# Kernel tuning notes

Hardware: AMD Instinct MI355X
Metric: run time of the kernel (lower is better)

## Reference

```python
import jax, jax.numpy as jnp
import numpy as np

B, S, DIN = 2, 2048, 1024
H = 16
DK = 1024   # dim_key_query_all
DV = 1024   # dim_value_all
DOUT = 1024
HEAD_SIZE = DK / H  # attention_head_size (float division in source)
LN_EPS = 1e-5


def setup_inputs() -> dict:
    key = jax.random.key(0)
    ks = jax.random.split(key, 12)
    s_in = 1.0 / np.sqrt(DIN)
    s_dv = 1.0 / np.sqrt(DV)
    return {
        "hidden_states": jax.random.normal(ks[0], (B, S, DIN), jnp.float32),
        "Wq": jax.random.uniform(ks[1], (DK, DIN), jnp.float32, -s_in, s_in),
        "Wk": jax.random.uniform(ks[2], (DK, DIN), jnp.float32, -s_in, s_in),
        "Wcb": jax.random.uniform(ks[3], (H, DIN), jnp.float32, -s_in, s_in),
        "Wv": jax.random.uniform(ks[4], (DV, DIN), jnp.float32, -s_in, s_in),
        "bv": jax.random.uniform(ks[5], (DV,), jnp.float32, -s_in, s_in),
        "mixing": 0.2 * jax.random.normal(ks[6], (H, DK), jnp.float32),
        "Wd": jax.random.uniform(ks[7], (DOUT, DV), jnp.float32, -s_dv, s_dv),
        "bd": jax.random.uniform(ks[8], (DOUT,), jnp.float32, -s_dv, s_dv),
        "gamma": jnp.ones((DV,), jnp.float32),
        "beta": jnp.zeros((DV,), jnp.float32),
    }


def reference(hidden_states, Wq, Wk, Wcb, Wv, bv, mixing, Wd, bd, gamma, beta):
    x = hidden_states  # [B, S, DIN]; self-attention: from == to
    q = jnp.einsum('bsd,kd->bsk', x, Wq)  # [B,S,DK]
    k = jnp.einsum('bsd,kd->bsk', x, Wk)  # [B,S,DK]
    # scores[b,h,i,j] = sum_c q[b,i,c]*mixing[h,c]*k[b,j,c]
    scores = jnp.einsum('bic,hc,bjc->bhij', q, mixing, k)
    cb = jnp.einsum('bjd,hd->bhj', x, Wcb)  # content bias [B,H,S]
    scores = scores + cb[:, :, None, :]
    scores = scores / jnp.sqrt(jnp.asarray(HEAD_SIZE, scores.dtype))
    probs = jax.nn.softmax(scores, axis=-1)  # dropout p=0.0 -> identity
    v = jnp.einsum('bsd,vd->bsv', x, Wv) + bv  # [B,S,DV]
    v = v.reshape(B, S, H, DV // H)
    ctx = jnp.einsum('bhij,bjhv->bihv', probs, v).reshape(B, S, DV)
    out = jnp.einsum('bsv,ov->bso', ctx, Wd) + bd
    res = x + out
    mu = jnp.mean(res, axis=-1, keepdims=True)
    var = jnp.var(res, axis=-1, keepdims=True)
    out = (res - mu) * jax.lax.rsqrt(var + LN_EPS) * gamma + beta
    return (out,)
```

## Files before the change

### kernel.cpp

```cpp
#include <hip/hip_runtime.h>
#include <cstddef>
#include <cstdint>

#define B_    2
#define S_    2048
#define DIN_  1024
#define H_    16
#define DK_   1024
#define DV_   1024
#define DH_   64
#define DOUT_ 1024
#define M_    (B_ * S_)

typedef __attribute__((ext_vector_type(8)))  short short8;
typedef __attribute__((ext_vector_type(4)))  float float4v;
typedef __attribute__((ext_vector_type(16))) float float16v;
typedef _Float16 half8v __attribute__((ext_vector_type(8)));

__device__ __forceinline__ float bf16s_to_f(short s) {
  union { unsigned int u; float f; } cv;
  cv.u = ((unsigned int)(unsigned short)s) << 16;
  return cv.f;
}
__device__ __forceinline__ short f_to_bf16s(float f) {
  union { float f; unsigned int u; } cv;
  cv.f = f;
  unsigned int u = cv.u + 0x7FFFu + ((cv.u >> 16) & 1u);
  return (short)(u >> 16);
}
__device__ __forceinline__ short f_to_f16s(float f) {
  union { _Float16 h; short s; } cv;
  cv.h = (_Float16)f;
  return cv.s;
}
__device__ __forceinline__ unsigned pkrtz_u32(float a, float b) {
  union { __fp16 __attribute__((ext_vector_type(2))) h2; unsigned u; } cv;
  cv.h2 = __builtin_amdgcn_cvt_pkrtz(a, b);
  return cv.u;
}
__device__ __forceinline__ void gll16(const void* g, void* l) {
  __builtin_amdgcn_global_load_lds(
      (const __attribute__((address_space(1))) unsigned int*)g,
      (__attribute__((address_space(3))) unsigned int*)l, 16, 0, 0);
}

__global__ __launch_bounds__(256) void cast_kernel(const float* __restrict__ in,
                                                   short* __restrict__ out, int n4) {
  int i = blockIdx.x * 256 + threadIdx.x;
  if (i >= n4) return;
  float4 v = ((const float4*)in)[i];
  union { ushort4 u; short s[4]; } o;
  o.s[0] = f_to_bf16s(v.x); o.s[1] = f_to_bf16s(v.y);
  o.s[2] = f_to_bf16s(v.z); o.s[3] = f_to_bf16s(v.w);
  ((ushort4*)out)[i] = o.u;
}

__global__ __launch_bounds__(256) void cb_kernel(const float* __restrict__ x,
                                                 const float* __restrict__ Wcb,
                                                 float* __restrict__ CBs) {
  __shared__ float xs[DIN_];
  const int row = blockIdx.x;
  const int tid = threadIdx.x;
  #pragma unroll
  for (int it = 0; it < 4; ++it)
    xs[tid + it * 256] = x[(size_t)row * DIN_ + tid + it * 256];
  __syncthreads();
  const int lane = tid & 63, w = tid >> 6;
  const float SC = 0.125f * 1.44269504088896f;
  #pragma unroll
  for (int hh = 0; hh < 4; ++hh) {
    const int hidx = w * 4 + hh;
    float p = 0.f;
    for (int c = lane; c < DIN_; c += 64)
      p += xs[c] * Wcb[(size_t)hidx * DIN_ + c];
    #pragma unroll
    for (int mk = 1; mk < 64; mk <<= 1) p += __shfl_xor(p, mk);
    if (lane == 0) {
      const int bb = row / S_, ss = row % S_;
      CBs[((size_t)bb * H_ + hidx) * S_ + ss] = p * SC;
    }
  }
}

__global__ __launch_bounds__(256, 2) void gemm_nt(
    const short* __restrict__ A, const short* __restrict__ Bw,
    const float* __restrict__ bias, const float* __restrict__ resid,
    short* __restrict__ outb, float* __restrict__ outf, int mode) {
  const int KD = 1024, ND = 1024;
  __shared__ short As[64][136];
  __shared__ short Bs[64][136];
  const int tid  = threadIdx.x;
  const int lane = tid & 63;
  const int w    = tid >> 6;
  const int quad = lane >> 4;
  const int l16  = lane & 15;
  const int m0   = blockIdx.y * 64;
  const int n0   = blockIdx.x * 64;
  const int wm   = (w >> 1) * 32;
  const int wn   = (w & 1) * 32;
  const int srow = tid >> 2;
  const int sseg = (tid & 3) * 32;

  const float4v zero = {0.f, 0.f, 0.f, 0.f};
  float4v acc[2][2];
  acc[0][0] = zero; acc[0][1] = zero; acc[1][0] = zero; acc[1][1] = zero;

  for (int k0 = 0; k0 < KD; k0 += 128) {
    short8 ar[4], br[4];
    #pragma unroll
    for (int c = 0; c < 4; ++c) {
      ar[c] = *(const short8*)(A  + (size_t)(m0 + srow) * KD + k0 + sseg + c * 8);
      br[c] = *(const short8*)(Bw + (size_t)(n0 + srow) * KD + k0 + sseg + c * 8);
    }
    __syncthreads();
    #pragma unroll
    for (int c = 0; c < 4; ++c) {
      *(short8*)&As[srow][sseg + c * 8] = ar[c];
      *(short8*)&Bs[srow][sseg + c * 8] = br[c];
    }
    __syncthreads();
    #pragma unroll
    for (int ks = 0; ks < 4; ++ks) {
      short8 af0 = *(short8*)&As[wm + l16][ks * 32 + quad * 8];
      short8 af1 = *(short8*)&As[wm + 16 + l16][ks * 32 + quad * 8];
      short8 bg0 = *(short8*)&Bs[wn + l16][ks * 32 + quad * 8];
      short8 bg1 = *(short8*)&Bs[wn + 16 + l16][ks * 32 + quad * 8];
      acc[0][0] = __builtin_amdgcn_mfma_f32_16x16x32_bf16(af0, bg0, acc[0][0], 0, 0, 0);
      acc[0][1] = __builtin_amdgcn_mfma_f32_16x16x32_bf16(af0, bg1, acc[0][1], 0, 0, 0);
      acc[1][0] = __builtin_amdgcn_mfma_f32_16x16x32_bf16(af1, bg0, acc[1][0], 0, 0, 0);
      acc[1][1] = __builtin_amdgcn_mfma_f32_16x16x32_bf16(af1, bg1, acc[1][1], 0, 0, 0);
    }
  }

  #pragma unroll
  for (int mt = 0; mt < 2; ++mt)
    #pragma unroll
    for (int nt = 0; nt < 2; ++nt)
      #pragma unroll
      for (int r = 0; r < 4; ++r) {
        int row = m0 + wm + mt * 16 + quad * 4 + r;
        int col = n0 + wn + nt * 16 + l16;
        float v = acc[mt][nt][r];
        if (mode == 1 || mode == 5) v += bias[col];
        if (mode == 2)
          outf[(size_t)row * ND + col] = v + bias[col] + resid[(size_t)row * ND + col];
        else if (mode == 5) {
          int bb = row >> 11, ss = row & 2047;
          outb[((size_t)bb * DV_ + col) * S_ + ss] = f_to_f16s(v);
        } else if (mode == 4)
          outb[(size_t)row * ND + col] = f_to_f16s(v);
        else
          outb[(size_t)row * ND + col] = f_to_bf16s(v);
      }
}

__global__ __launch_bounds__(256, 2) void attn_kernel(
    const short* __restrict__ Qf, const short* __restrict__ Kf,
    const short* __restrict__ Vtf, const float* __restrict__ mixing,
    const float* __restrict__ CBs, short* __restrict__ ctxb) {
  __shared__ __align__(16) short KsF[2 * 128 * 64];
  __shared__ __align__(16) short Vt[64][136];
  __shared__ __align__(16) short mix_s[DK_];
  __shared__ float cb_s[128];

  const int tid  = threadIdx.x;
  const int lane = tid & 63;
  const int l32  = lane & 31;
  const int l1   = lane >> 5;
  const int w    = tid >> 6;

  const int F    = blockIdx.x;
  const int xcd  = F & 7, rest = F >> 3;
  const int b    = xcd >> 2;
  const int h    = (xcd & 3) * 4 + (rest & 3);
  const int i0   = (rest >> 2) * 128;

  const float SC = 0.125f * 1.44269504088896f;
  for (int c = tid; c < DK_; c += 256) {
    union { _Float16 h; short s; } cv;
    cv.h = (_Float16)(mixing[(size_t)h * DK_ + c] * SC);
    mix_s[c] = cv.s;
  }

  const int iq = i0 + w * 32 + l32;
  const short* qptr  = Qf + ((size_t)b * S_ + iq) * DK_;
  const short* kbase = Kf + (size_t)b * S_ * DK_;
  const short* vtb   = Vtf + ((size_t)b * DV_ + h * DH_) * S_;
  const float* cbp   = CBs + ((size_t)b * H_ + h) * S_;

  float16v accS[4], accO[2];
  #pragma unroll
  for (int g = 0; g < 2; ++g)
    #pragma unroll
    for (int r = 0; r < 16; ++r) accO[g][r] = 0.f;
  float m_run = -1e30f, l_run = 0.f;

  const int nrow = lane >> 3;
  const int dp8  = lane & 7;

  const int vrow = tid >> 2;
  const int vseg = (tid & 3) * 32;

  for (int j0 = 0; j0 < S_; j0 += 128) {
    short8 vreg[4];
    #pragma unroll
    for (int c = 0; c < 4; ++c)
      vreg[c] = *(const short8*)(vtb + (size_t)vrow * S_ + j0 + vseg + c * 8);
    float cbv = 0.f;
    if (tid < 128) cbv = cbp[j0 + tid];
    __syncthreads();
    #pragma unroll
    for (int c = 0; c < 4; ++c)
      *(short8*)&Vt[vrow][vseg + c * 8] = vreg[c];
    if (tid < 128) cb_s[tid] = cbv;

    #pragma unroll
    for (int cc = 0; cc < 4; ++cc) {
      const int n = w * 4 + cc;
      const int r = 8 * n + nrow;
      const int lchunk = dp8 ^ (r & 7);
      gll16(kbase + (size_t)(j0 + r) * DK_ + lchunk * 8, &KsF[n * 512]);
    }
    half8v qcur[4], qnext[4];
    #pragma unroll
    for (int ks = 0; ks < 4; ++ks) {
      qcur[ks] = *(const half8v*)(qptr + ks * 16 + l1 * 8);
      qnext[ks] = qcur[ks];
    }

    #pragma unroll
    for (int f = 0; f < 4; ++f)
      #pragma unroll
      for (int r = 0; r < 16; ++r) accS[f][r] = 0.f;

    __syncthreads();

    for (int t = 0; t < 16; ++t) {
      if (t < 15) {
        const int nb = (t + 1) & 1;
        #pragma unroll
        for (int cc = 0; cc < 4; ++cc) {
          const int n = w * 4 + cc;
          const int r = 8 * n + nrow;
          const int lchunk = dp8 ^ (r & 7);
          gll16(kbase + (size_t)(j0 + r) * DK_ + (t + 1) * 64 + lchunk * 8,
                &KsF[nb * 8192 + n * 512]);
        }
        #pragma unroll
        for (int ks = 0; ks < 4; ++ks)
          qnext[ks] = *(const half8v*)(qptr + (t + 1) * 64 + ks * 16 + l1 * 8);
      }
      const short* kb = &KsF[(t & 1) * 8192];
      __builtin_amdgcn_s_setprio(1);
      #pragma unroll
      for (int ks = 0; ks < 4; ++ks) {
        half8v mf = *(half8v*)&mix_s[t * 64 + ks * 16 + l1 * 8];
        half8v qm = qcur[ks] * mf;
        const int poff = (((2 * ks + l1) ^ (l32 & 7)) * 8) + l32 * 64;
        #pragma unroll
        for (int f = 0; f < 4; ++f) {
          half8v af = *(half8v*)&kb[f * 2048 + poff];
          accS[f] = __builtin_amdgcn_mfma_f32_32x32x16_f16(af, qm, accS[f], 0, 0, 0);
        }
      }
      __builtin_amdgcn_s_setprio(0);
      #pragma unroll
      for (int ks = 0; ks < 4; ++ks) qcur[ks] = qnext[ks];
      __syncthreads();
    }

    float tmax = -1e30f;
    #pragma unroll
    for (int f = 0; f < 4; ++f)
      #pragma unroll
      for (int q = 0; q < 4; ++q) {
        float4 cbq = *(float4*)&cb_s[f * 32 + q * 8 + l1 * 4];
        #pragma unroll
        for (int c = 0; c < 4; ++c) {
          accS[f][4 * q + c] += ((const float*)&cbq)[c];
          tmax = fmaxf(tmax, accS[f][4 * q + c]);
        }
      }
    tmax = fmaxf(tmax, __shfl_xor(tmax, 32));
    const float mnew = fmaxf(m_run, tmax);
    const float alpha = exp2f(m_run - mnew);
    float tsum = 0.f;
    #pragma unroll
    for (int f = 0; f < 4; ++f)
      #pragma unroll
      for (int r = 0; r < 16; ++r) {
        float pv = exp2f(accS[f][r] - mnew);
        accS[f][r] = pv;
        tsum += pv;
      }
    tsum += __shfl_xor(tsum, 32);
    l_run = l_run * alpha + tsum;
    m_run = mnew;
    #pragma unroll
    for (int g = 0; g < 2; ++g)
      #pragma unroll
      for (int r = 0; r < 16; ++r) accO[g][r] *= alpha;

    #pragma unroll
    for (int cpv = 0; cpv < 8; ++cpv) {
      const int t = cpv & 1, fp = cpv >> 1;
      float xo[4], yo[4], lo[4], hi[4];
      #pragma unroll
      for (int c = 0; c < 4; ++c) {
        xo[c] = __shfl_xor(accS[fp][8 * t + c], 32);
        yo[c] = __shfl_xor(accS[fp][8 * t + 4 + c], 32);
      }
      #pragma unroll
      for (int c = 0; c < 4; ++c) {
        lo[c] = l1 ? yo[c] : accS[fp][8 * t + c];
        hi[c] = l1 ? accS[fp][8 * t + 4 + c] : xo[c];
      }
      union { half8v v; unsigned u[4]; } pb;
      pb.u[0] = pkrtz_u32(lo[0], lo[1]);
      pb.u[1] = pkrtz_u32(lo[2], lo[3]);
      pb.u[2] = pkrtz_u32(hi[0], hi[1]);
      pb.u[3] = pkrtz_u32(hi[2], hi[3]);
      #pragma unroll
      for (int g = 0; g < 2; ++g) {
        half8v vf = *(half8v*)&Vt[g * 32 + l32][cpv * 16 + l1 * 8];
        accO[g] = __builtin_amdgcn_mfma_f32_32x32x16_f16(vf, pb.v, accO[g], 0, 0, 0);
      }
    }
  }

  const float rl = 1.0f / l_run;
  short* cbase = ctxb + ((size_t)b * S_ + iq) * DV_ + h * DH_;
  #pragma unroll
  for (int g = 0; g < 2; ++g)
    #pragma unroll
    for (int q = 0; q < 4; ++q) {
      const int dv = g * 32 + 8 * q + 4 * l1;
      union { ushort4 u4; short s[4]; } ov;
      #pragma unroll
      for (int r = 0; r < 4; ++r)
        ov.s[r] = f_to_bf16s(accO[g][4 * q + r] * rl);
      *(ushort4*)(cbase + dv) = ov.u4;
    }
}

__global__ __launch_bounds__(256) void ln_kernel(float* __restrict__ out,
                                                 const float* __restrict__ gamma,
                                                 const float* __restrict__ beta) {
  __shared__ float red[8];
  const int row = blockIdx.x;
  const int tid = threadIdx.x;
  float* p = out + (size_t)row * DOUT_;
  float4 v = ((const float4*)p)[tid];
  float s = v.x + v.y + v.z + v.w;
  #pragma unroll
  for (int mk = 1; mk < 64; mk <<= 1) s += __shfl_xor(s, mk);
  if ((tid & 63) == 0) red[tid >> 6] = s;
  __syncthreads();
  const float mean = (red[0] + red[1] + red[2] + red[3]) * (1.0f / 1024.0f);
  const float d0 = v.x - mean, d1 = v.y - mean, d2 = v.z - mean, d3 = v.w - mean;
  float sq = d0 * d0 + d1 * d1 + d2 * d2 + d3 * d3;
  #pragma unroll
  for (int mk = 1; mk < 64; mk <<= 1) sq += __shfl_xor(sq, mk);
  if ((tid & 63) == 0) red[4 + (tid >> 6)] = sq;
  __syncthreads();
  const float var = (red[4] + red[5] + red[6] + red[7]) * (1.0f / 1024.0f);
  const float rstd = rsqrtf(var + 1e-5f);
  float4 g = ((const float4*)gamma)[tid];
  float4 bt = ((const float4*)beta)[tid];
  float4 o;
  o.x = d0 * rstd * g.x + bt.x;
  o.y = d1 * rstd * g.y + bt.y;
  o.z = d2 * rstd * g.z + bt.z;
  o.w = d3 * rstd * g.w + bt.w;
  ((float4*)p)[tid] = o;
}

extern "C" void kernel_launch(void* const* d_in, const int* in_sizes, int n_in,
                              void* d_out, int out_size, void* d_ws, size_t ws_size,
                              hipStream_t stream) {
  (void)in_sizes; (void)n_in; (void)out_size; (void)ws_size;
  const float* x      = (const float*)d_in[0];
  const float* Wq     = (const float*)d_in[1];
  const float* Wk     = (const float*)d_in[2];
  const float* Wcb    = (const float*)d_in[3];
  const float* Wv     = (const float*)d_in[4];
  const float* bv     = (const float*)d_in[5];
  const float* mixing = (const float*)d_in[6];
  const float* Wd     = (const float*)d_in[7];
  const float* bd     = (const float*)d_in[8];
  const float* gamma  = (const float*)d_in[9];
  const float* beta   = (const float*)d_in[10];
  float* out = (float*)d_out;

  short* p = (short*)d_ws;
  short* xb   = p; p += (size_t)M_ * DIN_;
  short* Qf   = p; p += (size_t)M_ * DK_;
  short* Kf   = p; p += (size_t)M_ * DK_;
  short* Vtf  = p; p += (size_t)B_ * DV_ * S_;
  short* ctxb = p; p += (size_t)M_ * DV_;
  short* Wqb  = p; p += (size_t)DK_ * DIN_;
  short* Wkb  = p; p += (size_t)DK_ * DIN_;
  short* Wvb  = p; p += (size_t)DV_ * DIN_;
  short* Wdb  = p; p += (size_t)DOUT_ * DV_;
  float* CBs  = (float*)p;

  cast_kernel<<<dim3(M_ * DIN_ / 1024), 256, 0, stream>>>(x, xb, M_ * DIN_ / 4);
  cast_kernel<<<dim3(DK_ * DIN_ / 1024), 256, 0, stream>>>(Wq, Wqb, DK_ * DIN_ / 4);
  cast_kernel<<<dim3(DK_ * DIN_ / 1024), 256, 0, stream>>>(Wk, Wkb, DK_ * DIN_ / 4);
  cast_kernel<<<dim3(DV_ * DIN_ / 1024), 256, 0, stream>>>(Wv, Wvb, DV_ * DIN_ / 4);
  cast_kernel<<<dim3(DOUT_ * DV_ / 1024), 256, 0, stream>>>(Wd, Wdb, DOUT_ * DV_ / 4);
  cb_kernel<<<dim3(M_), 256, 0, stream>>>(x, Wcb, CBs);

  dim3 gg(DOUT_ / 64, M_ / 64);
  gemm_nt<<<gg, 256, 0, stream>>>(xb, Wqb, nullptr, nullptr, Qf, nullptr, 4);
  gemm_nt<<<gg, 256, 0, stream>>>(xb, Wkb, nullptr, nullptr, Kf, nullptr, 4);
  gemm_nt<<<gg, 256, 0, stream>>>(xb, Wvb, bv, nullptr, Vtf, nullptr, 5);

  attn_kernel<<<dim3(512), 256, 0, stream>>>(Qf, Kf, Vtf, mixing, CBs, ctxb);

  gemm_nt<<<gg, 256, 0, stream>>>(ctxb, Wdb, bd, x, nullptr, out, 2);
  ln_kernel<<<dim3(M_), 256, 0, stream>>>(out, gamma, beta);
}
```

Before: 642.3 us.

## Split attention along key dimension into two halves with merge kernel

Splits each attention block's key range into two halves (flash-decoding style), doubling the grid to 1024 blocks, and writes unnormalized fp32 partial outputs plus running max/sum that a new merge kernel combines into the bf16 context. It also halves the K LDS buffer, replaces async global-to-LDS loads with register-staged prefetch, and raises launch bounds to 4 waves per SIMD to increase occupancy. The aim is better CU utilisation and latency hiding, at the cost of extra partial-result global traffic, an extra kernel launch, and more barriers per K-chunk.

Result: slower. 1.318 ms (+105.3%).

```diff
diff --git a/kernel.cpp b/kernel.cpp
--- a/kernel.cpp
+++ b/kernel.cpp
@@ -37,11 +37,6 @@
   union { __fp16 __attribute__((ext_vector_type(2))) h2; unsigned u; } cv;
   cv.h2 = __builtin_amdgcn_cvt_pkrtz(a, b);
   return cv.u;
-}
-__device__ __forceinline__ void gll16(const void* g, void* l) {
-  __builtin_amdgcn_global_load_lds(
-      (const __attribute__((address_space(1))) unsigned int*)g,
-      (__attribute__((address_space(3))) unsigned int*)l, 16, 0, 0);
 }
 
 __global__ __launch_bounds__(256) void cast_kernel(const float* __restrict__ in,
@@ -154,11 +149,12 @@
       }
 }
 
-__global__ __launch_bounds__(256, 2) void attn_kernel(
+__global__ __launch_bounds__(256, 4) void attn_kernel(
     const short* __restrict__ Qf, const short* __restrict__ Kf,
     const short* __restrict__ Vtf, const float* __restrict__ mixing,
-    const float* __restrict__ CBs, short* __restrict__ ctxb) {
-  __shared__ __align__(16) short KsF[2 * 128 * 64];
+    const float* __restrict__ CBs, float* __restrict__ Opart,
+    float2* __restrict__ ML) {
+  __shared__ __align__(16) short KsF[128 * 64];
   __shared__ __align__(16) short Vt[64][136];
   __shared__ __align__(16) short mix_s[DK_];
   __shared__ float cb_s[128];
@@ -173,12 +169,13 @@
   const int xcd  = F & 7, rest = F >> 3;
   const int b    = xcd >> 2;
   const int h    = (xcd & 3) * 4 + (rest & 3);
-  const int i0   = (rest >> 2) * 128;
+  const int i0   = ((rest >> 2) & 15) * 128;
+  const int jh   = (rest >> 6) & 1;
 
   const float SC = 0.125f * 1.44269504088896f;
   for (int c = tid; c < DK_; c += 256) {
-    union { _Float16 h; short s; } cv;
-    cv.h = (_Float16)(mixing[(size_t)h * DK_ + c] * SC);
+    union { _Float16 hh; short s; } cv;
+    cv.hh = (_Float16)(mixing[(size_t)h * DK_ + c] * SC);
     mix_s[c] = cv.s;
   }
 
@@ -195,78 +192,73 @@
     for (int r = 0; r < 16; ++r) accO[g][r] = 0.f;
   float m_run = -1e30f, l_run = 0.f;
 
-  const int nrow = lane >> 3;
-  const int dp8  = lane & 7;
+  const int rbase = tid >> 3;
+  const int chn   = tid & 7;
+  const int physc = chn ^ (rbase & 7);
 
   const int vrow = tid >> 2;
   const int vseg = (tid & 3) * 32;
 
-  for (int j0 = 0; j0 < S_; j0 += 128) {
-    short8 vreg[4];
+  for (int jt = 0; jt < 8; ++jt) {
+    const int j0 = jh * 1024 + jt * 128;
+    short8 vreg[4], kreg[4];
     #pragma unroll
     for (int c = 0; c < 4; ++c)
       vreg[c] = *(const short8*)(vtb + (size_t)vrow * S_ + j0 + vseg + c * 8);
+    #pragma unroll
+    for (int c = 0; c < 4; ++c)
+      kreg[c] = *(const short8*)(kbase + (size_t)(j0 + rbase + 32 * c) * DK_ + chn * 8);
     float cbv = 0.f;
     if (tid < 128) cbv = cbp[j0 + tid];
     __syncthreads();
     #pragma unroll
+    for (int c = 0; c < 4; ++c) {
+      *(short8*)&Vt[vrow][vseg + c * 8] = vreg[c];
+      *(short8*)&KsF[(rbase + 32 * c) * 64 + physc * 8] = kreg[c];
+    }
+    if (tid < 128) cb_s[tid] = cbv;
+    #pragma unroll
     for (int c = 0; c < 4; ++c)
-      *(short8*)&Vt[vrow][vseg + c * 8] = vreg[c];
-    if (tid < 128) cb_s[tid] = cbv;
-
-    #pragma unroll
-    for (int cc = 0; cc < 4; ++cc) {
-      const int n = w * 4 + cc;
-      const int r = 8 * n + nrow;
-      const int lchunk = dp8 ^ (r & 7);
-      gll16(kbase + (size_t)(j0 + r) * DK_ + lchunk * 8, &KsF[n * 512]);
-    }
-    half8v qcur[4], qnext[4];
-    #pragma unroll
-    for (int ks = 0; ks < 4; ++ks) {
-      qcur[ks] = *(const half8v*)(qptr + ks * 16 + l1 * 8);
-      qnext[ks] = qcur[ks];
-    }
+      kreg[c] = *(const short8*)(kbase + (size_t)(j0 + rbase + 32 * c) * DK_ + 64 + chn * 8);
+    __syncthreads();
 
     #pragma unroll
     for (int f = 0; f < 4; ++f)
       #pragma unroll
       for (int r = 0; r < 16; ++r) accS[f][r] = 0.f;
 
-    __syncthreads();
-
     for (int t = 0; t < 16; ++t) {
-      if (t < 15) {
-        const int nb = (t + 1) & 1;
-        #pragma unroll
-        for (int cc = 0; cc < 4; ++cc) {
-          const int n = w * 4 + cc;
-          const int r = 8 * n + nrow;
-          const int lchunk = dp8 ^ (r & 7);
-          gll16(kbase + (size_t)(j0 + r) * DK_ + (t + 1) * 64 + lchunk * 8,
-                &KsF[nb * 8192 + n * 512]);
-        }
-        #pragma unroll
-        for (int ks = 0; ks < 4; ++ks)
-          qnext[ks] = *(const half8v*)(qptr + (t + 1) * 64 + ks * 16 + l1 * 8);
-      }
-      const short* kb = &KsF[(t & 1) * 8192];
+      half8v qm[4];
+      #pragma unroll
+      for (int ks = 0; ks < 4; ++ks) {
+        half8v qr = *(const half8v*)(qptr + t * 64 + ks * 16 + l1 * 8);
+        half8v mf = *(half8v*)&mix_s[t * 64 + ks * 16 + l1 * 8];
+        qm[ks] = qr * mf;
+      }
       __builtin_amdgcn_s_setprio(1);
       #pragma unroll
       for (int ks = 0; ks < 4; ++ks) {
-        half8v mf = *(half8v*)&mix_s[t * 64 + ks * 16 + l1 * 8];
-        half8v qm = qcur[ks] * mf;
-        const int poff = (((2 * ks + l1) ^ (l32 & 7)) * 8) + l32 * 64;
+        const int po = ((2 * ks + l1) ^ (l32 & 7)) * 8;
         #pragma unroll
         for (int f = 0; f < 4; ++f) {
-          half8v af = *(half8v*)&kb[f * 2048 + poff];
-          accS[f] = __builtin_amdgcn_mfma_f32_32x32x16_f16(af, qm, accS[f], 0, 0, 0);
+          half8v af = *(half8v*)&KsF[(f * 32 + l32) * 64 + po];
+          accS[f] = __builtin_amdgcn_mfma_f32_32x32x16_f16(af, qm[ks], accS[f], 0, 0, 0);
         }
       }
       __builtin_amdgcn_s_setprio(0);
-      #pragma unroll
-      for (int ks = 0; ks < 4; ++ks) qcur[ks] = qnext[ks];
-      __syncthreads();
+      if (t < 15) {
+        __syncthreads();
+        #pragma unroll
+        for (int c = 0; c < 4; ++c)
+          *(short8*)&KsF[(rbase + 32 * c) * 64 + physc * 8] = kreg[c];
+        if (t < 14) {
+          #pragma unroll
+          for (int c = 0; c < 4; ++c)
+            kreg[c] = *(const short8*)(kbase + (size_t)(j0 + rbase + 32 * c) * DK_ +
+                                       (t + 2) * 64 + chn * 8);
+        }
+        __syncthreads();
+      }
     }
 
     float tmax = -1e30f;
@@ -303,17 +295,17 @@
 
     #pragma unroll
     for (int cpv = 0; cpv < 8; ++cpv) {
-      const int t = cpv & 1, fp = cpv >> 1;
+      const int tt = cpv & 1, fp = cpv >> 1;
       float xo[4], yo[4], lo[4], hi[4];
       #pragma unroll
       for (int c = 0; c < 4; ++c) {
-        xo[c] = __shfl_xor(accS[fp][8 * t + c], 32);
-        yo[c] = __shfl_xor(accS[fp][8 * t + 4 + c], 32);
+        xo[c] = __shfl_xor(accS[fp][8 * tt + c], 32);
+        yo[c] = __shfl_xor(accS[fp][8 * tt + 4 + c], 32);
       }
       #pragma unroll
       for (int c = 0; c < 4; ++c) {
-        lo[c] = l1 ? yo[c] : accS[fp][8 * t + c];
-        hi[c] = l1 ? accS[fp][8 * t + 4 + c] : xo[c];
+        lo[c] = l1 ? yo[c] : accS[fp][8 * tt + c];
+        hi[c] = l1 ? accS[fp][8 * tt + 4 + c] : xo[c];
       }
       union { half8v v; unsigned u[4]; } pb;
       pb.u[0] = pkrtz_u32(lo[0], lo[1]);
@@ -328,19 +320,44 @@
     }
   }
 
-  const float rl = 1.0f / l_run;
-  short* cbase = ctxb + ((size_t)b * S_ + iq) * DV_ + h * DH_;
+  const size_t prow = (size_t)jh * 65536 + (size_t)(b * H_ + h) * S_ + iq;
+  float* opb = Opart + prow * 64;
   #pragma unroll
   for (int g = 0; g < 2; ++g)
     #pragma unroll
     for (int q = 0; q < 4; ++q) {
       const int dv = g * 32 + 8 * q + 4 * l1;
-      union { ushort4 u4; short s[4]; } ov;
-      #pragma unroll
-      for (int r = 0; r < 4; ++r)
-        ov.s[r] = f_to_bf16s(accO[g][4 * q + r] * rl);
-      *(ushort4*)(cbase + dv) = ov.u4;
-    }
+      float4 ov;
+      ov.x = accO[g][4 * q + 0]; ov.y = accO[g][4 * q + 1];
+      ov.z = accO[g][4 * q + 2]; ov.w = accO[g][4 * q + 3];
+      *(float4*)(opb + dv) = ov;
+    }
+  if (l1 == 0) {
+    float2 ml; ml.x = m_run; ml.y = l_run;
+    ML[prow] = ml;
+  }
+}
+
+__global__ __launch_bounds__(256) void merge_kernel(
+    const float* __restrict__ Opart, const float2* __restrict__ ML,
+    short* __restrict__ ctxb) {
+  const int gid = blockIdx.x * 256 + threadIdx.x;
+  const int row = gid >> 4;
+  const int p4  = (gid & 15) * 4;
+  const float2 ml0 = ML[row], ml1 = ML[65536 + row];
+  const float m  = fmaxf(ml0.x, ml1.x);
+  const float e0 = exp2f(ml0.x - m), e1 = exp2f(ml1.x - m);
+  const float rl = 1.0f / (ml0.y * e0 + ml1.y * e1);
+  const float4 o0 = *(const float4*)(Opart + (size_t)row * 64 + p4);
+  const float4 o1 = *(const float4*)(Opart + (size_t)(65536 + row) * 64 + p4);
+  const int bh = row >> 11, i = row & 2047;
+  const int bb = bh >> 4, hh = bh & 15;
+  union { ushort4 u4; short s[4]; } ov;
+  ov.s[0] = f_to_bf16s((o0.x * e0 + o1.x * e1) * rl);
+  ov.s[1] = f_to_bf16s((o0.y * e0 + o1.y * e1) * rl);
+  ov.s[2] = f_to_bf16s((o0.z * e0 + o1.z * e1) * rl);
+  ov.s[3] = f_to_bf16s((o0.w * e0 + o1.w * e1) * rl);
+  *(ushort4*)(ctxb + ((size_t)(bb * S_ + i)) * DV_ + hh * DH_ + p4) = ov.u4;
 }
 
 __global__ __launch_bounds__(256) void ln_kernel(float* __restrict__ out,
@@ -403,6 +420,8 @@
   short* Wvb  = p; p += (size_t)DV_ * DIN_;
   short* Wdb  = p; p += (size_t)DOUT_ * DV_;
   float* CBs  = (float*)p;
+  float* Opart = CBs + (size_t)B_ * H_ * S_;
+  float2* ML   = (float2*)(Opart + (size_t)2 * 65536 * 64);
 
   cast_kernel<<<dim3(M_ * DIN_ / 1024), 256, 0, stream>>>(x, xb, M_ * DIN_ / 4);
   cast_kernel<<<dim3(DK_ * DIN_ / 1024), 256, 0, stream>>>(Wq, Wqb, DK_ * DIN_ / 4);
@@ -416,7 +435,8 @@
   gemm_nt<<<gg, 256, 0, stream>>>(xb, Wkb, nullptr, nullptr, Kf, nullptr, 4);
   gemm_nt<<<gg, 256, 0, stream>>>(xb, Wvb, bv, nullptr, Vtf, nullptr, 5);
 
-  attn_kernel<<<dim3(512), 256, 0, stream>>>(Qf, Kf, Vtf, mixing, CBs, ctxb);
+  attn_kernel<<<dim3(1024), 256, 0, stream>>>(Qf, Kf, Vtf, mixing, CBs, Opart, ML);
+  merge_kernel<<<dim3(4096), 256, 0, stream>>>(Opart, ML, ctxb);
 
   gemm_nt<<<gg, 256, 0, stream>>>(ctxb, Wdb, bd, x, nullptr, out, 2);
   ln_kernel<<<dim3(M_), 256, 0, stream>>>(out, gamma, beta);
```

## Load GEMM tiles directly to LDS with XOR-swizzled layout

Applied to the files above, without the earlier changes.

Replaces the register-staged global-to-LDS copy in gemm_nt with direct global-load-to-LDS (gll16) into an unpadded, XOR-swizzled shared layout, and raises launch bounds to allow four blocks per CU. The intent is to cut VGPR pressure and staging instructions, avoid LDS bank conflicts without padding, and improve occupancy. It relies on a gll16 helper defined elsewhere and on the swizzle matching between write and read indexing. It gives up the register prefetch, so global loads now sit between the two barriers.

New measurement: 632.3 us. No clear change (-1.6%).

```diff
diff --git a/kernel.cpp b/kernel.cpp
--- a/kernel.cpp
+++ b/kernel.cpp
@@ -82,13 +82,13 @@
   }
 }
 
-__global__ __launch_bounds__(256, 2) void gemm_nt(
+__global__ __launch_bounds__(256, 4) void gemm_nt(
     const short* __restrict__ A, const short* __restrict__ Bw,
     const float* __restrict__ bias, const float* __restrict__ resid,
     short* __restrict__ outb, float* __restrict__ outf, int mode) {
   const int KD = 1024, ND = 1024;
-  __shared__ short As[64][136];
-  __shared__ short Bs[64][136];
+  __shared__ __align__(16) short As[64 * 128];
+  __shared__ __align__(16) short Bs[64 * 128];
   const int tid  = threadIdx.x;
   const int lane = tid & 63;
   const int w    = tid >> 6;
@@ -98,33 +98,32 @@
   const int n0   = blockIdx.x * 64;
   const int wm   = (w >> 1) * 32;
   const int wn   = (w & 1) * 32;
-  const int srow = tid >> 2;
-  const int sseg = (tid & 3) * 32;
+
+  const int drow = lane >> 4;
+  const int dp   = lane & 15;
 
   const float4v zero = {0.f, 0.f, 0.f, 0.f};
   float4v acc[2][2];
   acc[0][0] = zero; acc[0][1] = zero; acc[1][0] = zero; acc[1][1] = zero;
 
   for (int k0 = 0; k0 < KD; k0 += 128) {
-    short8 ar[4], br[4];
-    #pragma unroll
-    for (int c = 0; c < 4; ++c) {
-      ar[c] = *(const short8*)(A  + (size_t)(m0 + srow) * KD + k0 + sseg + c * 8);
-      br[c] = *(const short8*)(Bw + (size_t)(n0 + srow) * KD + k0 + sseg + c * 8);
-    }
     __syncthreads();
     #pragma unroll
-    for (int c = 0; c < 4; ++c) {
-      *(short8*)&As[srow][sseg + c * 8] = ar[c];
-      *(short8*)&Bs[srow][sseg + c * 8] = br[c];
+    for (int cc = 0; cc < 4; ++cc) {
+      const int n = w * 4 + cc;
+      const int r = 4 * n + drow;
+      const int l = dp ^ (r & 15);
+      gll16(A  + (size_t)(m0 + r) * KD + k0 + l * 8, &As[n * 512]);
+      gll16(Bw + (size_t)(n0 + r) * KD + k0 + l * 8, &Bs[n * 512]);
     }
     __syncthreads();
     #pragma unroll
     for (int ks = 0; ks < 4; ++ks) {
-      short8 af0 = *(short8*)&As[wm + l16][ks * 32 + quad * 8];
-      short8 af1 = *(short8*)&As[wm + 16 + l16][ks * 32 + quad * 8];
-      short8 bg0 = *(short8*)&Bs[wn + l16][ks * 32 + quad * 8];
-      short8 bg1 = *(short8*)&Bs[wn + 16 + l16][ks * 32 + quad * 8];
+      const int ca = ((ks * 4 + quad) ^ l16) * 8;
+      short8 af0 = *(short8*)&As[(wm + l16) * 128 + ca];
+      short8 af1 = *(short8*)&As[(wm + 16 + l16) * 128 + ca];
+      short8 bg0 = *(short8*)&Bs[(wn + l16) * 128 + ca];
+      short8 bg1 = *(short8*)&Bs[(wn + 16 + l16) * 128 + ca];
       acc[0][0] = __builtin_amdgcn_mfma_f32_16x16x32_bf16(af0, bg0, acc[0][0], 0, 0, 0);
       acc[0][1] = __builtin_amdgcn_mfma_f32_16x16x32_bf16(af0, bg1, acc[0][1], 0, 0, 0);
       acc[1][0] = __builtin_amdgcn_mfma_f32_16x16x32_bf16(af1, bg0, acc[1][0], 0, 0, 0);
```
